# Kernel tuning notes

Measured on AMD Instinct MI355X. Metric: run time of the kernel, lower is better.

The kernel has to match this reference:

```python
import jax, jax.numpy as jnp
import numpy as np

V, D, H, L, FF, B, S = 32000, 1024, 16, 4, 4096, 2, 1024
DK = D // H
STD = 0.02


def setup_inputs() -> dict:
    key = jax.random.key(0)
    ks = jax.random.split(key, 9)
    emb = jax.random.normal(ks[0], (V, D), jnp.float32) * STD
    w_qkv = jax.random.normal(ks[1], (L, D, 3 * D), jnp.float32) * STD
    w_o = jax.random.normal(ks[2], (L, D, D), jnp.float32) * STD
    w_gate = jax.random.normal(ks[3], (L, D, FF), jnp.float32) * STD
    w_up = jax.random.normal(ks[4], (L, D, FF), jnp.float32) * STD
    w_down = jax.random.normal(ks[5], (L, FF, D), jnp.float32) * STD
    norm1_w = jnp.ones((L, D), jnp.float32)
    norm2_w = jnp.ones((L, D), jnp.float32)
    final_norm_w = jnp.ones((D,), jnp.float32)
    input_ids = jax.random.randint(ks[6], (B, S), 0, V, dtype=jnp.int32)
    return dict(input_ids=input_ids, emb=emb, w_qkv=w_qkv, w_o=w_o,
                norm1_w=norm1_w, norm2_w=norm2_w,
                w_gate=w_gate, w_up=w_up, w_down=w_down,
                final_norm_w=final_norm_w)


def _rms(x, w, eps=1e-8):
    return w * x / jnp.sqrt(jnp.mean(x * x, axis=-1, keepdims=True) + eps)


def _rope_factor(seq_len, dk):
    # original: x_rope = x*cos + x*sin with cos/sin of shape [S, dk/2]
    # (duplicated along the feature dim to make the broadcast well-defined)
    pos = jnp.arange(seq_len, dtype=jnp.float32)
    freqs = jnp.exp(jnp.arange(0, dk, 2, dtype=jnp.float32) * (-jnp.log(10000.0) / dk))
    ang = pos[:, None] * freqs[None, :]                     # [S, dk/2]
    c = jnp.cos(ang); s = jnp.sin(ang)
    return jnp.concatenate([c, c], -1) + jnp.concatenate([s, s], -1)  # [S, dk]


def reference(input_ids, emb, w_qkv, w_o, norm1_w, norm2_w, w_gate, w_up, w_down, final_norm_w):
    b, s = input_ids.shape
    d = emb.shape[1]
    x = emb[input_ids] * jnp.sqrt(jnp.float32(d))           # [B,S,D]
    rope = _rope_factor(s, DK)                              # [S,DK]
    causal = jnp.tril(jnp.ones((s, s), bool))
    scale = 1.0 / jnp.sqrt(jnp.float32(DK))

    def block(x, p):
        wqkv, wo, n1, n2, wg, wu, wd = p
        nx = _rms(x, n1)
        qkv = (nx @ wqkv).reshape(b, s, 3, H, DK).transpose(2, 0, 3, 1, 4)  # [3,B,H,S,DK]
        q, k, v = qkv[0], qkv[1], qkv[2]
        q = q * rope
        k = k * rope
        scores = jnp.einsum('bhsd,bhtd->bhst', q, k) * scale
        scores = jnp.where(causal, scores, jnp.float32(-1e9))
        attn = jax.nn.softmax(scores, axis=-1)
        o = jnp.einsum('bhst,bhtd->bhsd', attn, v)
        o = o.transpose(0, 2, 1, 3).reshape(b, s, d)
        x = x + o @ wo
        nx = _rms(x, n2)
        ff = (jax.nn.silu(nx @ wg) * (nx @ wu)) @ wd
        return x + ff, None

    x, _ = jax.lax.scan(block, x, (w_qkv, w_o, norm1_w, norm2_w, w_gate, w_up, w_down))
    x = _rms(x, final_norm_w)
    logits = x @ emb.T                                      # tied lm_head
    return logits
```

## Files before the change

### kernel.cpp

```cpp
#include <hip/hip_runtime.h>
#include <hip/hip_bf16.h>
#include <math.h>

#define B_ 2
#define S_ 1024
#define D_ 1024
#define H_ 16
#define DK_ 64
#define L_ 4
#define FF_ 4096
#define V_ 32000
#define NT (B_*S_)

typedef __attribute__((ext_vector_type(8))) short short8v;
typedef __attribute__((ext_vector_type(4))) float floatx4;
typedef __hip_bfloat16 bf16;

__device__ inline float b2f(unsigned short u) {
  unsigned v = ((unsigned)u) << 16;
  float f; __builtin_memcpy(&f, &v, 4); return f;
}
__device__ inline unsigned short f2bu(float f) {
  bf16 h = __float2bfloat16(f);
  unsigned short u; __builtin_memcpy(&u, &h, 2); return u;
}

__global__ __launch_bounds__(256) void k_embed(const int* __restrict__ ids,
    const float* __restrict__ emb, float* __restrict__ x) {
  int i = blockIdx.x*256 + threadIdx.x;
  if (i >= NT*D_) return;
  int tok = i >> 10;
  int d = i & 1023;
  x[i] = emb[(size_t)ids[tok]*D_ + d] * 32.0f;
}

__global__ __launch_bounds__(256) void k_rms(const float* __restrict__ x,
    const float* __restrict__ w, bf16* __restrict__ o) {
  int row = blockIdx.x;
  const float* xr = x + (size_t)row*D_;
  float s = 0.f;
  for (int d = threadIdx.x; d < D_; d += 256) { float v = xr[d]; s += v*v; }
  for (int off = 32; off; off >>= 1) s += __shfl_down(s, off);
  __shared__ float red[4];
  __shared__ float inv_s;
  int wid = threadIdx.x >> 6;
  if ((threadIdx.x & 63) == 0) red[wid] = s;
  __syncthreads();
  if (threadIdx.x == 0) {
    float t = red[0]+red[1]+red[2]+red[3];
    inv_s = 1.0f / sqrtf(t * (1.0f/D_) + 1e-8f);
  }
  __syncthreads();
  float inv = inv_s;
  bf16* orow = o + (size_t)row*D_;
  for (int d = threadIdx.x; d < D_; d += 256) orow[d] = __float2bfloat16(w[d]*xr[d]*inv);
}

__global__ __launch_bounds__(256) void k_transpose_cast(const float* __restrict__ src,
    bf16* __restrict__ dst, int K, int N) {
  __shared__ float t[32][33];
  int k0 = blockIdx.y*32, n0 = blockIdx.x*32;
  int tr = threadIdx.x >> 5, tc = threadIdx.x & 31;
  #pragma unroll
  for (int i=0;i<4;i++)
    t[tr + i*8][tc] = src[(size_t)(k0 + tr + i*8)*N + n0 + tc];
  __syncthreads();
  #pragma unroll
  for (int i=0;i<4;i++)
    dst[(size_t)(n0 + tr + i*8)*K + k0 + tc] = __float2bfloat16(t[tc][tr + i*8]);
}

__global__ __launch_bounds__(256) void k_cast4(const float* __restrict__ s,
    bf16* __restrict__ d, int n4) {
  int i = blockIdx.x*256 + threadIdx.x;
  if (i >= n4) return;
  float4 v = ((const float4*)s)[i];
  ushort4 o;
  o.x = f2bu(v.x); o.y = f2bu(v.y); o.z = f2bu(v.z); o.w = f2bu(v.w);
  ((ushort4*)d)[i] = o;
}

template<bool RES, bool OUTBF>
__global__ __launch_bounds__(256) void k_mfma_gemm_bt(
    const bf16* __restrict__ A, const bf16* __restrict__ Bt,
    const float* __restrict__ res, void* __restrict__ Cout,
    int M, int N, int K) {
  __shared__ bf16 As[128*32];
  __shared__ bf16 Bs[128*32];
  const int tid  = threadIdx.x;
  const int lane = tid & 63;
  const int wave = tid >> 6;
  const int wm = (wave >> 1) * 64;
  const int wn = (wave & 1) * 64;
  const int bm = blockIdx.y * 128;
  const int bn = blockIdx.x * 128;

  floatx4 acc[4][4] = {};

  for (int k0 = 0; k0 < K; k0 += 32) {
    #pragma unroll
    for (int c = 0; c < 2; ++c) {
      int e = (c*256 + tid) * 8;
      int row = e >> 5, col = e & 31;
      const bf16* ga = A  + (size_t)(bm + row)*K + k0 + col;
      const bf16* gb = Bt + (size_t)(bn + row)*K + k0 + col;
      int ldsoff = (c*256 + wave*64) * 8;
      __builtin_amdgcn_global_load_lds(
        (const __attribute__((address_space(1))) void*)ga,
        (__attribute__((address_space(3))) void*)(As + ldsoff), 16, 0, 0);
      __builtin_amdgcn_global_load_lds(
        (const __attribute__((address_space(1))) void*)gb,
        (__attribute__((address_space(3))) void*)(Bs + ldsoff), 16, 0, 0);
    }
    __syncthreads();
    const int r = lane & 15, kc = lane >> 4;
    short8v a[4], b[4];
    #pragma unroll
    for (int i = 0; i < 4; ++i) {
      a[i] = *(const short8v*)(As + (size_t)(wm + i*16 + r)*32 + kc*8);
      b[i] = *(const short8v*)(Bs + (size_t)(wn + i*16 + r)*32 + kc*8);
    }
    #pragma unroll
    for (int i = 0; i < 4; ++i)
      #pragma unroll
      for (int j = 0; j < 4; ++j)
        acc[i][j] = __builtin_amdgcn_mfma_f32_16x16x32_bf16(a[i], b[j], acc[i][j], 0, 0, 0);
    __syncthreads();
  }

  const int cn = lane & 15, rq = lane >> 4;
  #pragma unroll
  for (int i=0;i<4;i++) {
    #pragma unroll
    for (int j=0;j<4;j++) {
      #pragma unroll
      for (int rr=0; rr<4; ++rr) {
        int grow = bm + wm + i*16 + rq*4 + rr;
        int gcol = bn + wn + j*16 + cn;
        float v = acc[i][j][rr];
        if (RES) v += res[(size_t)grow*N + gcol];
        if (OUTBF) ((bf16*)Cout)[(size_t)grow*N + gcol] = __float2bfloat16(v);
        else       ((float*)Cout)[(size_t)grow*N + gcol] = v;
      }
    }
  }
}

__global__ __launch_bounds__(256) void k_rope_bf(bf16* __restrict__ qkv) {
  int i = blockIdx.x*256 + threadIdx.x;
  if (i >= NT*2048) return;
  int tok = i >> 11;
  int c = i & 2047;
  int j = c & 31;
  int s = tok & (S_-1);
  float freq = expf((float)j * -0.28782313662425574f);
  float ang = (float)s * freq;
  size_t idx = (size_t)tok*3072 + c;
  unsigned short* p = (unsigned short*)qkv;
  p[idx] = f2bu(b2f(p[idx]) * (cosf(ang) + sinf(ang)));
}

__global__ __launch_bounds__(256) void k_fattn(const bf16* __restrict__ qkvb,
    bf16* __restrict__ outb) {
  const unsigned short* qkv = (const unsigned short*)qkvb;
  const int qt = 15 - blockIdx.x;
  const int h = blockIdx.y, b = blockIdx.z;
  const int tid = threadIdx.x, lane = tid & 63, w = tid >> 6;
  const int g = lane >> 4, qn = lane & 15;

  __shared__ unsigned short Ks[64*64];
  __shared__ unsigned short Vt[64*64];
  __shared__ unsigned short Ps[4*16*64];

  const int q0 = qt * 64;
  const int qw0 = q0 + w*16;

  short8v qf[2];
  {
    const unsigned short* qp = qkv + ((size_t)(b*S_ + qw0 + qn))*3072 + h*DK_ + g*8;
    qf[0] = *(const short8v*)qp;
    qf[1] = *(const short8v*)(qp + 32);
  }

  floatx4 o_acc[4] = {};
  float m_run = -1e30f, l_run = 0.f;

  const int ntile = qt + 1;
  for (int it = 0; it < ntile; ++it) {
    const int t0 = it*64;

    {
      const int trow = w*8 + (lane>>3);
      const int d16 = (lane&7) ^ (trow&7);
      #pragma unroll
      for (int c = 0; c < 2; ++c) {
        const unsigned short* gk = qkv + ((size_t)(b*S_ + t0 + c*32 + trow))*3072
                                   + 1024 + h*DK_ + d16*8;
        __builtin_amdgcn_global_load_lds(
          (const __attribute__((address_space(1))) void*)gk,
          (__attribute__((address_space(3))) void*)(Ks + c*2048 + w*512), 16, 0, 0);
      }
    }
    #pragma unroll
    for (int c = 0; c < 2; ++c) {
      int idx = c*256 + tid;
      int t = idx >> 3;
      int d0 = (idx & 7)*8;
      short8v vv = *(const short8v*)(qkv + ((size_t)(b*S_ + t0 + t))*3072 + 2048 + h*DK_ + d0);
      #pragma unroll
      for (int jj = 0; jj < 8; ++jj) {
        int d = d0 + jj;
        int slot = ((t>>3) ^ (d&7) ^ ((d>>3)&7)) & 7;
        Vt[d*64 + slot*8 + (t&7)] = (unsigned short)vv[jj];
      }
    }
    __syncthreads();

    floatx4 st[4];
    #pragma unroll
    for (int f = 0; f < 4; ++f) {
      st[f] = (floatx4){0.f,0.f,0.f,0.f};
      int t = f*16 + qn;
      #pragma unroll
      for (int ks = 0; ks < 2; ++ks) {
        int slot = ((ks*4 + g) ^ (t&7)) & 7;
        short8v kf = *(const short8v*)(Ks + t*64 + slot*8);
        st[f] = __builtin_amdgcn_mfma_f32_16x16x32_bf16(kf, qf[ks], st[f], 0,0,0);
      }
    }

    const bool diag = (it == qt);
    float sc[4][4];
    #pragma unroll
    for (int f = 0; f < 4; ++f)
      #pragma unroll
      for (int r = 0; r < 4; ++r) {
        float v = st[f][r]*0.125f;
        if (diag) {
          int tl = f*16 + g*4 + r;
          if (tl > w*16 + qn) v = -1e30f;
        }
        sc[f][r] = v;
      }
    float mx = -1e30f;
    #pragma unroll
    for (int f = 0; f < 4; ++f)
      #pragma unroll
      for (int r = 0; r < 4; ++r) mx = fmaxf(mx, sc[f][r]);
    mx = fmaxf(mx, __shfl_xor(mx, 16));
    mx = fmaxf(mx, __shfl_xor(mx, 32));
    float m_new = fmaxf(m_run, mx);
    float corr = __expf(m_run - m_new);
    m_run = m_new;
    float ls = 0.f;
    #pragma unroll
    for (int f = 0; f < 4; ++f)
      #pragma unroll
      for (int r = 0; r < 4; ++r) {
        float p = __expf(sc[f][r] - m_new);
        sc[f][r] = p;
        ls += p;
      }
    ls += __shfl_xor(ls, 16);
    ls += __shfl_xor(ls, 32);
    l_run = l_run*corr + ls;

    unsigned short* Pw = Ps + w*1024;
    #pragma unroll
    for (int f = 0; f < 4; ++f) {
      unsigned int lo = (unsigned int)f2bu(sc[f][0]) | ((unsigned int)f2bu(sc[f][1]) << 16);
      unsigned int hi = (unsigned int)f2bu(sc[f][2]) | ((unsigned int)f2bu(sc[f][3]) << 16);
      int c16 = f*2 + (g>>1);
      int slot = (c16 ^ (qn&7)) & 7;
      *(uint2*)((char*)Pw + qn*128 + slot*16 + (g&1)*8) = make_uint2(lo, hi);
    }

    #pragma unroll
    for (int r = 0; r < 4; ++r) {
      float cr = __shfl(corr, g*4 + r);
      #pragma unroll
      for (int fd = 0; fd < 4; ++fd) o_acc[fd][r] *= cr;
    }

    short8v pf[2];
    #pragma unroll
    for (int ks = 0; ks < 2; ++ks) {
      int slot = ((ks*4 + g) ^ (qn&7)) & 7;
      pf[ks] = *(const short8v*)(Pw + qn*64 + slot*8);
    }
    #pragma unroll
    for (int fd = 0; fd < 4; ++fd) {
      int d = fd*16 + qn;
      #pragma unroll
      for (int ks = 0; ks < 2; ++ks) {
        int slot = ((ks*4 + g) ^ (d&7) ^ ((d>>3)&7)) & 7;
        short8v vf = *(const short8v*)(Vt + d*64 + slot*8);
        o_acc[fd] = __builtin_amdgcn_mfma_f32_16x16x32_bf16(pf[ks], vf, o_acc[fd], 0,0,0);
      }
    }
    __syncthreads();
  }

  float linv = 1.0f / l_run;
  #pragma unroll
  for (int r = 0; r < 4; ++r) {
    float li = __shfl(linv, g*4 + r);
    int row = qw0 + g*4 + r;
    bf16* op = outb + (size_t)(b*S_ + row)*D_ + h*DK_ + qn;
    #pragma unroll
    for (int fd = 0; fd < 4; ++fd)
      op[fd*16] = __float2bfloat16(o_acc[fd][r] * li);
  }
}

__global__ __launch_bounds__(256) void k_silumul_bf(bf16* __restrict__ g,
    const bf16* __restrict__ u, int n) {
  int i = blockIdx.x*256 + threadIdx.x;
  if (i < n) {
    unsigned short* gp = (unsigned short*)g;
    float v = b2f(gp[i]);
    float sg = v / (1.0f + expf(-v));
    gp[i] = f2bu(sg * b2f(((const unsigned short*)u)[i]));
  }
}

extern "C" void kernel_launch(void* const* d_in, const int* in_sizes, int n_in,
                              void* d_out, int out_size, void* d_ws, size_t ws_size,
                              hipStream_t stream) {
  (void)in_sizes; (void)n_in; (void)out_size; (void)ws_size;
  const int*   ids  = (const int*)d_in[0];
  const float* emb  = (const float*)d_in[1];
  const float* wqkv = (const float*)d_in[2];
  const float* wo   = (const float*)d_in[3];
  const float* n1   = (const float*)d_in[4];
  const float* n2   = (const float*)d_in[5];
  const float* wg   = (const float*)d_in[6];
  const float* wu   = (const float*)d_in[7];
  const float* wd   = (const float*)d_in[8];
  const float* fnw  = (const float*)d_in[9];
  float* out = (float*)d_out;

  char* ws = (char*)d_ws;
  float* x      = (float*)ws;                                   ws += (size_t)NT*D_*4;
  bf16*  nx_bf  = (bf16*)ws;                                    ws += (size_t)NT*D_*2;
  bf16*  att_bf = (bf16*)ws;                                    ws += (size_t)NT*D_*2;
  bf16*  shared = (bf16*)ws;                                    ws += (size_t)2*NT*FF_*2;
  bf16*  emb_bf = (bf16*)ws;                                    ws += (size_t)V_*D_*2;
  bf16*  qkv_bf = shared;
  bf16*  g_bf   = shared;
  bf16*  u_bf   = shared + (size_t)NT*FF_;

  bf16* wsc = (bf16*)d_out;
  bf16* wqkv_t = wsc;
  bf16* wo_t   = wqkv_t + (size_t)L_*3*D_*D_;
  bf16* wg_t   = wo_t   + (size_t)L_*D_*D_;
  bf16* wu_t   = wg_t   + (size_t)L_*D_*FF_;
  bf16* wd_t   = wu_t   + (size_t)L_*D_*FF_;

  dim3 blk(256);

  for (int l = 0; l < L_; ++l) {
    dim3 gq(3*D_/32, D_/32);
    k_transpose_cast<<<gq, blk, 0, stream>>>(wqkv + (size_t)l*D_*3*D_, wqkv_t + (size_t)l*3*D_*D_, D_, 3*D_);
    dim3 go(D_/32, D_/32);
    k_transpose_cast<<<go, blk, 0, stream>>>(wo + (size_t)l*D_*D_, wo_t + (size_t)l*D_*D_, D_, D_);
    dim3 gg(FF_/32, D_/32);
    k_transpose_cast<<<gg, blk, 0, stream>>>(wg + (size_t)l*D_*FF_, wg_t + (size_t)l*D_*FF_, D_, FF_);
    k_transpose_cast<<<gg, blk, 0, stream>>>(wu + (size_t)l*D_*FF_, wu_t + (size_t)l*D_*FF_, D_, FF_);
    dim3 gd(D_/32, FF_/32);
    k_transpose_cast<<<gd, blk, 0, stream>>>(wd + (size_t)l*FF_*D_, wd_t + (size_t)l*D_*FF_, FF_, D_);
  }
  k_cast4<<<(V_*D_/4 + 255)/256, blk, 0, stream>>>(emb, emb_bf, V_*D_/4);

  k_embed<<<(NT*D_+255)/256, blk, 0, stream>>>(ids, emb, x);

  for (int l = 0; l < L_; ++l) {
    k_rms<<<NT, blk, 0, stream>>>(x, n1 + (size_t)l*D_, nx_bf);
    dim3 gqkv(3*D_/128, NT/128);
    k_mfma_gemm_bt<false,true><<<gqkv, blk, 0, stream>>>(nx_bf, wqkv_t + (size_t)l*3*D_*D_, nullptr, qkv_bf, NT, 3*D_, D_);
    k_rope_bf<<<(NT*2048+255)/256, blk, 0, stream>>>(qkv_bf);
    dim3 gattn(16, H_, B_);
    k_fattn<<<gattn, blk, 0, stream>>>(qkv_bf, att_bf);
    dim3 go(D_/128, NT/128);
    k_mfma_gemm_bt<true,false><<<go, blk, 0, stream>>>(att_bf, wo_t + (size_t)l*D_*D_, x, x, NT, D_, D_);
    k_rms<<<NT, blk, 0, stream>>>(x, n2 + (size_t)l*D_, nx_bf);
    dim3 gff(FF_/128, NT/128);
    k_mfma_gemm_bt<false,true><<<gff, blk, 0, stream>>>(nx_bf, wg_t + (size_t)l*D_*FF_, nullptr, g_bf, NT, FF_, D_);
    k_mfma_gemm_bt<false,true><<<gff, blk, 0, stream>>>(nx_bf, wu_t + (size_t)l*D_*FF_, nullptr, u_bf, NT, FF_, D_);
    k_silumul_bf<<<(NT*FF_+255)/256, blk, 0, stream>>>(g_bf, u_bf, NT*FF_);
    dim3 gd2(D_/128, NT/128);
    k_mfma_gemm_bt<true,false><<<gd2, blk, 0, stream>>>(g_bf, wd_t + (size_t)l*D_*FF_, x, x, NT, D_, FF_);
  }
  k_rms<<<NT, blk, 0, stream>>>(x, fnw, nx_bf);
  dim3 glog(V_/128, NT/128);
  k_mfma_gemm_bt<false,false><<<glog, blk, 0, stream>>>(nx_bf, emb_bf, nullptr, out, NT, V_, D_);
}
```

Before: 1.576 ms.

## Fuse RoPE and SiLU-mul into GEMM epilogues, remap GEMM grid, widen transpose

Folds the RoPE scaling into the QKV GEMM epilogue and the SiLU(gate)*up product into the up-projection GEMM epilogue. This removes the separate rope and silu-mul kernels and the u buffer round trip. The GEMM launch becomes a 1D grid remapped so consecutive workgroups on the same XCD share an N tile, for better L2 reuse. The weight transpose-cast now uses 64x64 tiles with float4 loads and ushort4 stores. The gate output is read and overwritten in place by the up GEMM; this is safe only because each output element is read and written by the same thread.

```diff
diff --git a/kernel.cpp b/kernel.cpp
--- a/kernel.cpp
+++ b/kernel.cpp
@@ -58,16 +58,27 @@
 
 __global__ __launch_bounds__(256) void k_transpose_cast(const float* __restrict__ src,
     bf16* __restrict__ dst, int K, int N) {
-  __shared__ float t[32][33];
-  int k0 = blockIdx.y*32, n0 = blockIdx.x*32;
-  int tr = threadIdx.x >> 5, tc = threadIdx.x & 31;
+  __shared__ float t[64][65];
+  int k0 = blockIdx.y*64, n0 = blockIdx.x*64;
+  int r  = threadIdx.x >> 4;
+  int c4 = (threadIdx.x & 15)*4;
   #pragma unroll
-  for (int i=0;i<4;i++)
-    t[tr + i*8][tc] = src[(size_t)(k0 + tr + i*8)*N + n0 + tc];
+  for (int i = 0; i < 4; ++i) {
+    float4 v = *(const float4*)(src + (size_t)(k0 + r + i*16)*N + n0 + c4);
+    t[r+i*16][c4] = v.x; t[r+i*16][c4+1] = v.y;
+    t[r+i*16][c4+2] = v.z; t[r+i*16][c4+3] = v.w;
+  }
   __syncthreads();
+  int nn = threadIdx.x >> 2;
+  int kc = threadIdx.x & 3;
   #pragma unroll
-  for (int i=0;i<4;i++)
-    dst[(size_t)(n0 + tr + i*8)*K + k0 + tc] = __float2bfloat16(t[tc][tr + i*8]);
+  for (int i = 0; i < 4; ++i) {
+    int kk = kc*4 + i*16;
+    ushort4 o;
+    o.x = f2bu(t[kk][nn]);   o.y = f2bu(t[kk+1][nn]);
+    o.z = f2bu(t[kk+2][nn]); o.w = f2bu(t[kk+3][nn]);
+    *(ushort4*)(dst + (size_t)(n0+nn)*K + k0 + kk) = o;
+  }
 }
 
 __global__ __launch_bounds__(256) void k_cast4(const float* __restrict__ s,
@@ -80,11 +91,20 @@
   ((ushort4*)d)[i] = o;
 }
 
-template<bool RES, bool OUTBF>
+template<int EPI, bool OUTBF>
 __global__ __launch_bounds__(256) void k_mfma_gemm_bt(
     const bf16* __restrict__ A, const bf16* __restrict__ Bt,
-    const float* __restrict__ res, void* __restrict__ Cout,
+    const void* __restrict__ aux, void* __restrict__ Cout,
     int M, int N, int K) {
+  const int NM = M >> 7, NN = N >> 7;
+  const int wg = blockIdx.x;
+  const int grp = wg >> 3, xcd = wg & 7;
+  const int mi = grp % NM;
+  const int ni = xcd + 8*(grp / NM);
+  if (ni >= NN) return;
+  const int bm = mi * 128;
+  const int bn = ni * 128;
+
   __shared__ bf16 As[128*32];
   __shared__ bf16 Bs[128*32];
   const int tid  = threadIdx.x;
@@ -92,8 +112,6 @@
   const int wave = tid >> 6;
   const int wm = (wave >> 1) * 64;
   const int wn = (wave & 1) * 64;
-  const int bm = blockIdx.y * 128;
-  const int bn = blockIdx.x * 128;
 
   floatx4 acc[4][4] = {};
 
@@ -133,31 +151,40 @@
   for (int i=0;i<4;i++) {
     #pragma unroll
     for (int j=0;j<4;j++) {
+      const int gcol = bn + wn + j*16 + cn;
+      float freq = 0.f;
+      if constexpr (EPI==2) {
+        if (gcol < 2048)
+          freq = expf((float)(gcol & 31) * -0.28782313662425574f);
+      }
       #pragma unroll
       for (int rr=0; rr<4; ++rr) {
-        int grow = bm + wm + i*16 + rq*4 + rr;
-        int gcol = bn + wn + j*16 + cn;
+        const int grow = bm + wm + i*16 + rq*4 + rr;
+        const size_t off = (size_t)grow*N + gcol;
         float v = acc[i][j][rr];
-        if (RES) v += res[(size_t)grow*N + gcol];
-        if (OUTBF) ((bf16*)Cout)[(size_t)grow*N + gcol] = __float2bfloat16(v);
-        else       ((float*)Cout)[(size_t)grow*N + gcol] = v;
-      }
-    }
-  }
-}
-
-__global__ __launch_bounds__(256) void k_rope_bf(bf16* __restrict__ qkv) {
-  int i = blockIdx.x*256 + threadIdx.x;
-  if (i >= NT*2048) return;
-  int tok = i >> 11;
-  int c = i & 2047;
-  int j = c & 31;
-  int s = tok & (S_-1);
-  float freq = expf((float)j * -0.28782313662425574f);
-  float ang = (float)s * freq;
-  size_t idx = (size_t)tok*3072 + c;
-  unsigned short* p = (unsigned short*)qkv;
-  p[idx] = f2bu(b2f(p[idx]) * (cosf(ang) + sinf(ang)));
+        if constexpr (EPI==1) v += ((const float*)aux)[off];
+        if constexpr (EPI==2) {
+          if (gcol < 2048) {
+            float sn, cs;
+            sincosf((float)(grow & 1023) * freq, &sn, &cs);
+            v *= (cs + sn);
+          }
+        }
+        if constexpr (EPI==3) {
+          float gv = b2f(((const unsigned short*)aux)[off]);
+          v *= gv / (1.0f + expf(-gv));
+        }
+        if constexpr (OUTBF) ((bf16*)Cout)[off] = __float2bfloat16(v);
+        else                 ((float*)Cout)[off] = v;
+      }
+    }
+  }
+}
+
+static inline int remap_grid(int M, int N) {
+  int NM = M >> 7, NN = N >> 7;
+  int NN8 = (NN + 7) & ~7;
+  return NM * NN8;
 }
 
 __global__ __launch_bounds__(256) void k_fattn(const bf16* __restrict__ qkvb,
@@ -310,17 +337,6 @@
     #pragma unroll
     for (int fd = 0; fd < 4; ++fd)
       op[fd*16] = __float2bfloat16(o_acc[fd][r] * li);
-  }
-}
-
-__global__ __launch_bounds__(256) void k_silumul_bf(bf16* __restrict__ g,
-    const bf16* __restrict__ u, int n) {
-  int i = blockIdx.x*256 + threadIdx.x;
-  if (i < n) {
-    unsigned short* gp = (unsigned short*)g;
-    float v = b2f(gp[i]);
-    float sg = v / (1.0f + expf(-v));
-    gp[i] = f2bu(sg * b2f(((const unsigned short*)u)[i]));
   }
 }
 
@@ -348,7 +364,6 @@
   bf16*  emb_bf = (bf16*)ws;                                    ws += (size_t)V_*D_*2;
   bf16*  qkv_bf = shared;
   bf16*  g_bf   = shared;
-  bf16*  u_bf   = shared + (size_t)NT*FF_;
 
   bf16* wsc = (bf16*)d_out;
   bf16* wqkv_t = wsc;
@@ -360,14 +375,14 @@
   dim3 blk(256);
 
   for (int l = 0; l < L_; ++l) {
-    dim3 gq(3*D_/32, D_/32);
+    dim3 gq(3*D_/64, D_/64);
     k_transpose_cast<<<gq, blk, 0, stream>>>(wqkv + (size_t)l*D_*3*D_, wqkv_t + (size_t)l*3*D_*D_, D_, 3*D_);
-    dim3 go(D_/32, D_/32);
+    dim3 go(D_/64, D_/64);
     k_transpose_cast<<<go, blk, 0, stream>>>(wo + (size_t)l*D_*D_, wo_t + (size_t)l*D_*D_, D_, D_);
-    dim3 gg(FF_/32, D_/32);
+    dim3 gg(FF_/64, D_/64);
     k_transpose_cast<<<gg, blk, 0, stream>>>(wg + (size_t)l*D_*FF_, wg_t + (size_t)l*D_*FF_, D_, FF_);
     k_transpose_cast<<<gg, blk, 0, stream>>>(wu + (size_t)l*D_*FF_, wu_t + (size_t)l*D_*FF_, D_, FF_);
-    dim3 gd(D_/32, FF_/32);
+    dim3 gd(D_/64, FF_/64);
     k_transpose_cast<<<gd, blk, 0, stream>>>(wd + (size_t)l*FF_*D_, wd_t + (size_t)l*D_*FF_, FF_, D_);
   }
   k_cast4<<<(V_*D_/4 + 255)/256, blk, 0, stream>>>(emb, emb_bf, V_*D_/4);
@@ -376,22 +391,21 @@
 
   for (int l = 0; l < L_; ++l) {
     k_rms<<<NT, blk, 0, stream>>>(x, n1 + (size_t)l*D_, nx_bf);
-    dim3 gqkv(3*D_/128, NT/128);
-    k_mfma_gemm_bt<false,true><<<gqkv, blk, 0, stream>>>(nx_bf, wqkv_t + (size_t)l*3*D_*D_, nullptr, qkv_bf, NT, 3*D_, D_);
-    k_rope_bf<<<(NT*2048+255)/256, blk, 0, stream>>>(qkv_bf);
+    k_mfma_gemm_bt<2,true><<<remap_grid(NT,3*D_), blk, 0, stream>>>(
+        nx_bf, wqkv_t + (size_t)l*3*D_*D_, nullptr, qkv_bf, NT, 3*D_, D_);
     dim3 gattn(16, H_, B_);
     k_fattn<<<gattn, blk, 0, stream>>>(qkv_bf, att_bf);
-    dim3 go(D_/128, NT/128);
-    k_mfma_gemm_bt<true,false><<<go, blk, 0, stream>>>(att_bf, wo_t + (size_t)l*D_*D_, x, x, NT, D_, D_);
+    k_mfma_gemm_bt<1,false><<<remap_grid(NT,D_), blk, 0, stream>>>(
+        att_bf, wo_t + (size_t)l*D_*D_, x, x, NT, D_, D_);
     k_rms<<<NT, blk, 0, stream>>>(x, n2 + (size_t)l*D_, nx_bf);
-    dim3 gff(FF_/128, NT/128);
-    k_mfma_gemm_bt<false,true><<<gff, blk, 0, stream>>>(nx_bf, wg_t + (size_t)l*D_*FF_, nullptr, g_bf, NT, FF_, D_);
-    k_mfma_gemm_bt<false,true><<<gff, blk, 0, stream>>>(nx_bf, wu_t + (size_t)l*D_*FF_, nullptr, u_bf, NT, FF_, D_);
-    k_silumul_bf<<<(NT*FF_+255)/256, blk, 0, stream>>>(g_bf, u_bf, NT*FF_);
-    dim3 gd2(D_/128, NT/128);
-    k_mfma_gemm_bt<true,false><<<gd2, blk, 0, stream>>>(g_bf, wd_t + (size_t)l*D_*FF_, x, x, NT, D_, FF_);
+    k_mfma_gemm_bt<0,true><<<remap_grid(NT,FF_), blk, 0, stream>>>(
+        nx_bf, wg_t + (size_t)l*D_*FF_, nullptr, g_bf, NT, FF_, D_);
+    k_mfma_gemm_bt<3,true><<<remap_grid(NT,FF_), blk, 0, stream>>>(
+        nx_bf, wu_t + (size_t)l*D_*FF_, g_bf, g_bf, NT, FF_, D_);
+    k_mfma_gemm_bt<1,false><<<remap_grid(NT,D_), blk, 0, stream>>>(
+        g_bf, wd_t + (size_t)l*D_*FF_, x, x, NT, D_, FF_);
   }
   k_rms<<<NT, blk, 0, stream>>>(x, fnw, nx_bf);
-  dim3 glog(V_/128, NT/128);
-  k_mfma_gemm_bt<false,false><<<glog, blk, 0, stream>>>(nx_bf, emb_bf, nullptr, out, NT, V_, D_);
-}
+  k_mfma_gemm_bt<0,false><<<remap_grid(NT,V_), blk, 0, stream>>>(
+      nx_bf, emb_bf, nullptr, out, NT, V_, D_);
+}
```

Result: no change. 1.600 ms (+1.6%).
